# Kernel tuning notes

Hardware: AMD Instinct MI355X
Metric: run time of the kernel (lower is better)

The kernel has to match this reference:

```python
import jax, jax.numpy as jnp
import numpy as np

HIDDEN = 1024
HEADS = 16
HEAD_DIM = HIDDEN // HEADS
GAMMA = 0.5
B, S = 2, 2048


def setup_inputs() -> dict:
    key = jax.random.key(0)
    ks = jax.random.split(key, 9)
    sc = 1.0 / np.sqrt(HIDDEN)
    x = jax.random.normal(ks[0], (B, S, HIDDEN), dtype=jnp.float32)
    attn_mask = jnp.zeros((S, S), dtype=bool)  # True = masked; all-False here
    Wq = jax.random.normal(ks[1], (HIDDEN, HIDDEN), dtype=jnp.float32) * sc
    bq = jnp.zeros((HIDDEN,), dtype=jnp.float32)
    Wk = jax.random.normal(ks[2], (HIDDEN, HIDDEN), dtype=jnp.float32) * sc
    bk = jnp.zeros((HIDDEN,), dtype=jnp.float32)
    Wv = jax.random.normal(ks[3], (HIDDEN, HIDDEN), dtype=jnp.float32) * sc
    bv = jnp.zeros((HIDDEN,), dtype=jnp.float32)
    Wo = jax.random.normal(ks[4], (HIDDEN, HIDDEN), dtype=jnp.float32) * sc
    bo = jnp.zeros((HIDDEN,), dtype=jnp.float32)
    return {"x": x, "attn_mask": attn_mask, "Wq": Wq, "bq": bq,
            "Wk": Wk, "bk": bk, "Wv": Wv, "bv": bv, "Wo": Wo, "bo": bo}


def reference(x, attn_mask, Wq, bq, Wk, bk, Wv, bv, Wo, bo):
    Bn, Sn, _ = x.shape
    # projections (torch Linear: x @ W.T + b), reshape to [B, H, S, Dh]
    def proj(W, b):
        y = x @ W.T + b
        return y.reshape(Bn, Sn, HEADS, HEAD_DIM).transpose(0, 2, 1, 3)
    q, k, v = proj(Wq, bq), proj(Wk, bk), proj(Wv, bv)
    scores = jnp.einsum('bhqd,bhkd->bhqk', q, k) / np.sqrt(HEAD_DIM)
    # diversity bias: cosine similarity of raw x (F.normalize eps=1e-12)
    normed = x / jnp.maximum(jnp.linalg.norm(x, axis=-1, keepdims=True), 1e-12)
    sim = jnp.einsum('bqd,bkd->bqk', normed, normed)
    scores = scores - GAMMA * sim[:, None, :, :]
    scores = jnp.where(attn_mask[None, None, :, :], -jnp.inf, scores)
    probs = jax.nn.softmax(scores, axis=-1)
    ctx = jnp.einsum('bhqk,bhkd->bhqd', probs, v)
    ctx = ctx.transpose(0, 2, 1, 3).reshape(Bn, Sn, HIDDEN)
    return ctx @ Wo.T + bo
```

## Files before the change

kernel.cpp:

```cpp
#include <hip/hip_runtime.h>

#define HID 1024
#define SEQ 2048
#define NB 2
#define NH 16
#define HD 64

#define C1 0.1803368801111204f
#define C2 0.7213475204444817f

typedef __attribute__((ext_vector_type(8))) short bf16x8;
typedef __attribute__((ext_vector_type(8))) unsigned short u16x8;
typedef __attribute__((ext_vector_type(4))) float f32x4;

__device__ __forceinline__ unsigned short f2bf(float f) {
  unsigned u = __builtin_bit_cast(unsigned, f);
  u += 0x7fffu + ((u >> 16) & 1u);
  return (unsigned short)(u >> 16);
}
__device__ __forceinline__ float bf2f(unsigned short u) {
  return __builtin_bit_cast(float, ((unsigned)u) << 16);
}
__device__ __forceinline__ float fexp2(float x) {
  float r;
  asm("v_exp_f32 %0, %1" : "=v"(r) : "v"(x));
  return r;
}

#define GLOAD16(gsrc, ldst)                                                     \
  __builtin_amdgcn_global_load_lds(                                             \
      (const __attribute__((address_space(1))) void*)(gsrc),                    \
      (__attribute__((address_space(3))) void*)(ldst), 16, 0, 0)

__global__ __launch_bounds__(256) void prep_kernel(
    const float* __restrict__ x,
    const float* __restrict__ Wq, const float* __restrict__ Wk,
    const float* __restrict__ Wv, const float* __restrict__ Wo,
    unsigned short* __restrict__ Wb,
    unsigned short* __restrict__ xb, unsigned short* __restrict__ nxb) {
  int tid = threadIdx.x;
  if (blockIdx.x < 2048) {
    int i = blockIdx.x * 256 + tid;
    const int per = (HID * HID) / 8;
    int m = i / per;
    const float* sp = (m == 0) ? Wq : (m == 1) ? Wk : (m == 2) ? Wv : Wo;
    int j = (i - m * per) * 8;
    const float4* p = reinterpret_cast<const float4*>(sp + j);
    float4 a = p[0], b = p[1];
    u16x8 o;
    o[0] = f2bf(a.x); o[1] = f2bf(a.y); o[2] = f2bf(a.z); o[3] = f2bf(a.w);
    o[4] = f2bf(b.x); o[5] = f2bf(b.y); o[6] = f2bf(b.z); o[7] = f2bf(b.w);
    *reinterpret_cast<u16x8*>(Wb + (size_t)i * 8) = o;
  } else {
    int row = blockIdx.x - 2048;
    const float4 v = reinterpret_cast<const float4*>(x + (size_t)row * HID)[tid];
    float ss = v.x * v.x + v.y * v.y + v.z * v.z + v.w * v.w;
#pragma unroll
    for (int off = 32; off; off >>= 1) ss += __shfl_xor(ss, off, 64);
    __shared__ float wsum[4];
    if ((tid & 63) == 0) wsum[tid >> 6] = ss;
    __syncthreads();
    float tot = wsum[0] + wsum[1] + wsum[2] + wsum[3];
    float inv = 1.0f / fmaxf(sqrtf(tot), 1e-12f);
    ushort4 a, b;
    a.x = f2bf(v.x); a.y = f2bf(v.y); a.z = f2bf(v.z); a.w = f2bf(v.w);
    b.x = f2bf(v.x * inv); b.y = f2bf(v.y * inv);
    b.z = f2bf(v.z * inv); b.w = f2bf(v.w * inv);
    reinterpret_cast<ushort4*>(xb  + (size_t)row * HID)[tid] = a;
    reinterpret_cast<ushort4*>(nxb + (size_t)row * HID)[tid] = b;
  }
}

#define GEMM_K_LOOP64                                                           \
  for (int kt = 0; kt < 16; ++kt) {                                             \
    _Pragma("unroll")                                                           \
    for (int j = 0; j < 4; j++) {                                               \
      GLOAD16(Ab + (size_t)j * 32 * K + kt * 64, &As[j * 2048 + wid * 512]);    \
      GLOAD16(Bb + (size_t)j * 32 * K + kt * 64, &Bs[j * 2048 + wid * 512]);    \
    }                                                                           \
    __syncthreads();                                                            \
    _Pragma("unroll")                                                           \
    for (int h = 0; h < 2; h++) {                                               \
      bf16x8 af[4], bfr[4];                                                     \
      _Pragma("unroll")                                                         \
      for (int i = 0; i < 4; i++) {                                             \
        af[i]  = *reinterpret_cast<const bf16x8*>(                              \
            &As[(wr * 64 + i * 16 + lr) * 64 + ((((h << 2) + g) ^ (lr & 7)) << 3)]); \
        bfr[i] = *reinterpret_cast<const bf16x8*>(                              \
            &Bs[(wc * 64 + i * 16 + lr) * 64 + ((((h << 2) + g) ^ (lr & 7)) << 3)]); \
      }                                                                         \
      _Pragma("unroll")                                                         \
      for (int i = 0; i < 4; i++)                                               \
        _Pragma("unroll")                                                       \
        for (int j = 0; j < 4; j++)                                             \
          acc[i][j] = __builtin_amdgcn_mfma_f32_16x16x32_bf16(af[i], bfr[j], acc[i][j], 0, 0, 0); \
    }                                                                           \
    __syncthreads();                                                            \
  }

__global__ __launch_bounds__(256) void mega_gemm(
    const unsigned short* __restrict__ xb, const unsigned short* __restrict__ nxb,
    const unsigned short* __restrict__ Wb,
    unsigned short* __restrict__ QK, unsigned short* __restrict__ VT,
    unsigned short* __restrict__ D2,
    const float* __restrict__ bq, const float* __restrict__ bk,
    const float* __restrict__ bv, const unsigned char* __restrict__ mask) {
  const int K = HID;
  int bid = blockIdx.x;
  int mode, m0, n0;
  const unsigned short *A, *B;
  size_t zoff = 0;
  if (bid < 512) {
    mode = 0; m0 = (bid >> 4) * 128; n0 = (bid & 15) * 128;
    A = xb; B = Wb;
  } else if (bid < 768) {
    mode = 3; int t = bid - 512; m0 = (t >> 5) * 128; n0 = (t & 31) * 128;
    A = Wb + (size_t)2 * HID * HID; B = xb;
  } else {
    mode = 1; int t = bid - 768; int z = 0;
    if (t >= 136) { z = 1; t -= 136; }
    int a = (int)((sqrtf(8.0f * t + 1.0f) - 1.0f) * 0.5f);
    while (a * (a + 1) / 2 > t) a--;
    while ((a + 1) * (a + 2) / 2 <= t) a++;
    int bI = t - a * (a + 1) / 2;
    m0 = bI * 128; n0 = a * 128;
    A = nxb + (size_t)z * SEQ * HID; B = A;
    zoff = (size_t)z * SEQ * SEQ;
  }

  __shared__ __align__(16) unsigned short As[128 * 64];
  __shared__ __align__(16) unsigned short Bs[128 * 64];
  int tid = threadIdx.x, lane = tid & 63, wid = tid >> 6;
  int g = lane >> 4, lr = lane & 15;
  int wr = wid >> 1, wc = wid & 1;
  const unsigned short* Ab = A + (size_t)(m0 + wid * 8 + (lane >> 3)) * K
                             + (((lane & 7) ^ (lane >> 3)) << 3);
  const unsigned short* Bb = B + (size_t)(n0 + wid * 8 + (lane >> 3)) * K
                             + (((lane & 7) ^ (lane >> 3)) << 3);

  f32x4 acc[4][4] = {};
  GEMM_K_LOOP64

#pragma unroll
  for (int i = 0; i < 4; i++)
#pragma unroll
    for (int j = 0; j < 4; j++) {
      int col = n0 + wc * 64 + j * 16 + lr;
#pragma unroll
      for (int r = 0; r < 4; r++) {
        int row = m0 + wr * 64 + i * 16 + 4 * g + r;
        float v = acc[i][j][r];
        if (mode == 0) {
          const float* bp = (col < 1024) ? bq : bk;
          QK[(size_t)row * 2048 + col] = f2bf(v + bp[col & 1023]);
        } else if (mode == 3) {
          VT[(size_t)row * 4096 + col] = f2bf(v + bv[row]);
        } else {
          float t1 = -C2 * v + (mask[(size_t)row * SEQ + col] ? -1e30f : 0.0f);
          D2[zoff + (size_t)row * SEQ + col] = f2bf(t1);
          if (m0 != n0) {
            float t2 = -C2 * v + (mask[(size_t)col * SEQ + row] ? -1e30f : 0.0f);
            D2[zoff + (size_t)col * SEQ + row] = f2bf(t2);
          }
        }
      }
    }
}

__global__ __launch_bounds__(256) void gemm_out(
    const unsigned short* __restrict__ A, const unsigned short* __restrict__ B,
    float* __restrict__ C, const float* __restrict__ b0) {
  const int K = HID;
  __shared__ __align__(16) unsigned short As[128 * 64];
  __shared__ __align__(16) unsigned short Bs[128 * 64];
  int tid = threadIdx.x, lane = tid & 63, wid = tid >> 6;
  int g = lane >> 4, lr = lane & 15;
  int wr = wid >> 1, wc = wid & 1;
  int m0 = blockIdx.y * 128, n0 = blockIdx.x * 128;
  const unsigned short* Ab = A + (size_t)(m0 + wid * 8 + (lane >> 3)) * K
                             + (((lane & 7) ^ (lane >> 3)) << 3);
  const unsigned short* Bb = B + (size_t)(n0 + wid * 8 + (lane >> 3)) * K
                             + (((lane & 7) ^ (lane >> 3)) << 3);

  f32x4 acc[4][4] = {};
  GEMM_K_LOOP64

#pragma unroll
  for (int i = 0; i < 4; i++)
#pragma unroll
    for (int j = 0; j < 4; j++) {
      int col = n0 + wc * 64 + j * 16 + lr;
#pragma unroll
      for (int r = 0; r < 4; r++) {
        int row = m0 + wr * 64 + i * 16 + 4 * g + r;
        C[(size_t)row * HID + col] = acc[i][j][r] + b0[col];
      }
    }
}

__global__ __launch_bounds__(256, 4) void flash_kernel(
    const unsigned short* __restrict__ QK,
    const unsigned short* __restrict__ VT,
    const unsigned short* __restrict__ D2,
    unsigned short* __restrict__ ctxb) {
  int h = blockIdx.x, qt = blockIdx.y, b = blockIdx.z;
  int tid = threadIdx.x, wid = tid >> 6, lane = tid & 63;
  int g = lane >> 4, lr = lane & 15;
  __shared__ __align__(16) unsigned short Ks[2][64 * 64];
  __shared__ __align__(16) unsigned short Vt[2][64 * 64];
  const size_t ld = 2 * HID;
  const size_t bS = (size_t)b * SEQ;
  const int qbase = qt * 64 + wid * 16;

  const unsigned short* qp = QK + (bS + qbase + lr) * ld + h * HD + g * 8;
  bf16x8 qf0 = *reinterpret_cast<const bf16x8*>(qp);
  bf16x8 qf1 = *reinterpret_cast<const bf16x8*>(qp + 32);

  const int p0 = wid * 16 + (lane >> 3);
  const int key0 = ((p0 >> 5) & 1) * 32 + (((p0 >> 2) & 3) << 3)
                 + ((p0 >> 4) & 1) * 4 + (p0 & 3);
  const unsigned short* gK0 = QK + (bS + key0) * ld + HID + h * HD
                              + (((lane & 7) ^ (lane >> 3)) << 3);
  const unsigned short* gK1 = gK0 + 16 * ld;

  const unsigned short* gV0 = VT + (size_t)(h * HD + wid * 16 + (lane >> 3)) * (2 * SEQ)
                              + bS + (((lane & 7) ^ (lane >> 3)) << 3);
  const unsigned short* gV1 = gV0 + (size_t)8 * (2 * SEQ);

  const unsigned short* bD = D2 + (size_t)b * SEQ * SEQ
                             + (size_t)(qbase + lr) * SEQ + 8 * g;

  GLOAD16(gK0, &Ks[0][wid * 1024]);
  GLOAD16(gK1, &Ks[0][wid * 1024 + 512]);
  GLOAD16(gV0, &Vt[0][wid * 1024]);
  GLOAD16(gV1, &Vt[0][wid * 1024 + 512]);
  ushort4 bvc[4];
  bvc[0] = *reinterpret_cast<const ushort4*>(bD + 0);
  bvc[1] = *reinterpret_cast<const ushort4*>(bD + 4);
  bvc[2] = *reinterpret_cast<const ushort4*>(bD + 32);
  bvc[3] = *reinterpret_cast<const ushort4*>(bD + 36);
  __syncthreads();

  f32x4 acc[4] = {};
  f32x4 rsacc = {};
  const int kb0 = lr * 64 + ((g ^ (lr & 7)) << 3);
  bf16x8 ones;
#pragma unroll
  for (int i = 0; i < 8; i++) ones[i] = 0x3F80;

  for (int kt = 0; kt < 32; ++kt) {
    const int cb = kt & 1;
    const unsigned short* ks = &Ks[cb][0];
    const unsigned short* vt = &Vt[cb][0];
    ushort4 bvn[4];
    if (kt < 31) {
      GLOAD16(gK0 + (size_t)(kt + 1) * 64 * ld, &Ks[cb ^ 1][wid * 1024]);
      GLOAD16(gK1 + (size_t)(kt + 1) * 64 * ld, &Ks[cb ^ 1][wid * 1024 + 512]);
      GLOAD16(gV0 + (kt + 1) * 64, &Vt[cb ^ 1][wid * 1024]);
      GLOAD16(gV1 + (kt + 1) * 64, &Vt[cb ^ 1][wid * 1024 + 512]);
      const unsigned short* bn = bD + (kt + 1) * 64;
      bvn[0] = *reinterpret_cast<const ushort4*>(bn + 0);
      bvn[1] = *reinterpret_cast<const ushort4*>(bn + 4);
      bvn[2] = *reinterpret_cast<const ushort4*>(bn + 32);
      bvn[3] = *reinterpret_cast<const ushort4*>(bn + 36);
    }

    f32x4 s[4];
    __builtin_amdgcn_s_setprio(1);
#pragma unroll
    for (int kc = 0; kc < 4; kc++) {
      bf16x8 kf0 = *reinterpret_cast<const bf16x8*>(ks + kc * 1024 + kb0);
      bf16x8 kf1 = *reinterpret_cast<const bf16x8*>(ks + kc * 1024 + (kb0 ^ 32));
      f32x4 z = {};
      z = __builtin_amdgcn_mfma_f32_16x16x32_bf16(kf0, qf0, z, 0, 0, 0);
      s[kc] = __builtin_amdgcn_mfma_f32_16x16x32_bf16(kf1, qf1, z, 0, 0, 0);
    }
    __builtin_amdgcn_s_setprio(0);

    bf16x8 pa[2];
#pragma unroll
    for (int c2 = 0; c2 < 2; c2++) {
      float p0f = fexp2(fmaf(s[2 * c2][0], C1, bf2f(bvc[2 * c2].x)));
      float p1f = fexp2(fmaf(s[2 * c2][1], C1, bf2f(bvc[2 * c2].y)));
      float p2f = fexp2(fmaf(s[2 * c2][2], C1, bf2f(bvc[2 * c2].z)));
      float p3f = fexp2(fmaf(s[2 * c2][3], C1, bf2f(bvc[2 * c2].w)));
      float p4f = fexp2(fmaf(s[2 * c2 + 1][0], C1, bf2f(bvc[2 * c2 + 1].x)));
      float p5f = fexp2(fmaf(s[2 * c2 + 1][1], C1, bf2f(bvc[2 * c2 + 1].y)));
      float p6f = fexp2(fmaf(s[2 * c2 + 1][2], C1, bf2f(bvc[2 * c2 + 1].z)));
      float p7f = fexp2(fmaf(s[2 * c2 + 1][3], C1, bf2f(bvc[2 * c2 + 1].w)));
      uint4 W;
      W.x = __builtin_amdgcn_perm(__builtin_bit_cast(unsigned, p1f),
                                  __builtin_bit_cast(unsigned, p0f), 0x07060302u);
      W.y = __builtin_amdgcn_perm(__builtin_bit_cast(unsigned, p3f),
                                  __builtin_bit_cast(unsigned, p2f), 0x07060302u);
      W.z = __builtin_amdgcn_perm(__builtin_bit_cast(unsigned, p5f),
                                  __builtin_bit_cast(unsigned, p4f), 0x07060302u);
      W.w = __builtin_amdgcn_perm(__builtin_bit_cast(unsigned, p7f),
                                  __builtin_bit_cast(unsigned, p6f), 0x07060302u);
      pa[c2] = __builtin_bit_cast(bf16x8, W);
    }

    __builtin_amdgcn_s_setprio(1);
#pragma unroll
    for (int c2 = 0; c2 < 2; c2++) {
      rsacc = __builtin_amdgcn_mfma_f32_16x16x32_bf16(pa[c2], ones, rsacc, 0, 0, 0);
#pragma unroll
      for (int df = 0; df < 4; df++) {
        bf16x8 vf = *reinterpret_cast<const bf16x8*>(
            vt + (df * 16 + lr) * 64 + (((4 * c2 + g) ^ (lr & 7)) << 3));
        acc[df] = __builtin_amdgcn_mfma_f32_16x16x32_bf16(pa[c2], vf, acc[df], 0, 0, 0);
      }
    }
    __builtin_amdgcn_s_setprio(0);

    if (kt < 31) {
      bvc[0] = bvn[0]; bvc[1] = bvn[1]; bvc[2] = bvn[2]; bvc[3] = bvn[3];
    }
    __syncthreads();
  }
  float l0 = 1.0f / rsacc[0], l1 = 1.0f / rsacc[1];
  float l2 = 1.0f / rsacc[2], l3 = 1.0f / rsacc[3];
  unsigned short* op = ctxb + (bS + qbase + 4 * g) * HID + h * HD + lr;
#pragma unroll
  for (int df = 0; df < 4; df++) {
    op[0 * HID + df * 16] = f2bf(acc[df][0] * l0);
    op[1 * HID + df * 16] = f2bf(acc[df][1] * l1);
    op[2 * HID + df * 16] = f2bf(acc[df][2] * l2);
    op[3 * HID + df * 16] = f2bf(acc[df][3] * l3);
  }
}

extern "C" void kernel_launch(void* const* d_in, const int* in_sizes, int n_in,
                              void* d_out, int out_size, void* d_ws, size_t ws_size,
                              hipStream_t stream) {
  const float* x = (const float*)d_in[0];
  const unsigned char* mask = (const unsigned char*)d_in[1];
  const float* Wq = (const float*)d_in[2];
  const float* bq = (const float*)d_in[3];
  const float* Wk = (const float*)d_in[4];
  const float* bk = (const float*)d_in[5];
  const float* Wv = (const float*)d_in[6];
  const float* bv = (const float*)d_in[7];
  const float* Wo = (const float*)d_in[8];
  const float* bo = (const float*)d_in[9];
  float* out = (float*)d_out;

  char* ws = (char*)d_ws;
  const size_t MiB = 1024 * 1024;
  unsigned short* xb  = (unsigned short*)(ws + 0 * MiB);
  unsigned short* nxb = (unsigned short*)(ws + 8 * MiB);
  unsigned short* Wb  = (unsigned short*)(ws + 16 * MiB);
  unsigned short* QK  = (unsigned short*)(ws + 24 * MiB);
  unsigned short* VT  = (unsigned short*)(ws + 40 * MiB);
  unsigned short* D2  = (unsigned short*)(ws + 48 * MiB);
  unsigned short* ctx = (unsigned short*)(ws + 64 * MiB);

  prep_kernel<<<6144, 256, 0, stream>>>(x, Wq, Wk, Wv, Wo, Wb, xb, nxb);
  mega_gemm<<<1040, 256, 0, stream>>>(xb, nxb, Wb, QK, VT, D2, bq, bk, bv, mask);
  flash_kernel<<<dim3(NH, SEQ / 64, NB), 256, 0, stream>>>(QK, VT, D2, ctx);
  gemm_out<<<dim3(8, 32), 256, 0, stream>>>(
      ctx, Wb + (size_t)3 * HID * HID, out, bo);
}
```

Baseline: 204.7 us.

## Shrink GEMM K-tile to 32 and remap block IDs across XCDs

The shared GEMM K-loop now stages 32-wide K slices instead of 64, with a new XOR swizzle and per-wave LDS regions. This halves LDS use and may allow more resident blocks. Both mega_gemm and gemm_out also remap blockIdx so that consecutive tiles land on the same XCD (stride-8 interleave), which is meant to improve L2 reuse of shared A/B panels. The cost is twice as many barriers and a shorter MFMA run per K step.

```diff
diff --git a/kernel.cpp b/kernel.cpp
--- a/kernel.cpp
+++ b/kernel.cpp
@@ -71,30 +71,26 @@
   }
 }
 
-#define GEMM_K_LOOP64                                                           \
-  for (int kt = 0; kt < 16; ++kt) {                                             \
+#define GEMM_K_LOOP32                                                           \
+  for (int k0 = 0; k0 < K; k0 += 32) {                                          \
+    GLOAD16(Ab + k0, la);                                                       \
+    GLOAD16(Ab + 16 * K + k0, la + 512);                                        \
+    GLOAD16(Bb + k0, lb);                                                       \
+    GLOAD16(Bb + 16 * K + k0, lb + 512);                                        \
+    __syncthreads();                                                            \
+    bf16x8 af[4], bfr[4];                                                       \
     _Pragma("unroll")                                                           \
-    for (int j = 0; j < 4; j++) {                                               \
-      GLOAD16(Ab + (size_t)j * 32 * K + kt * 64, &As[j * 2048 + wid * 512]);    \
-      GLOAD16(Bb + (size_t)j * 32 * K + kt * 64, &Bs[j * 2048 + wid * 512]);    \
+    for (int i = 0; i < 4; i++) {                                               \
+      af[i]  = *reinterpret_cast<const bf16x8*>(                                \
+          &As[(wr * 64 + i * 16 + lr) * 32 + ((g ^ ((lr >> 1) & 3)) << 3)]);    \
+      bfr[i] = *reinterpret_cast<const bf16x8*>(                                \
+          &Bs[(wc * 64 + i * 16 + lr) * 32 + ((g ^ ((lr >> 1) & 3)) << 3)]);    \
     }                                                                           \
-    __syncthreads();                                                            \
     _Pragma("unroll")                                                           \
-    for (int h = 0; h < 2; h++) {                                               \
-      bf16x8 af[4], bfr[4];                                                     \
+    for (int i = 0; i < 4; i++)                                                 \
       _Pragma("unroll")                                                         \
-      for (int i = 0; i < 4; i++) {                                             \
-        af[i]  = *reinterpret_cast<const bf16x8*>(                              \
-            &As[(wr * 64 + i * 16 + lr) * 64 + ((((h << 2) + g) ^ (lr & 7)) << 3)]); \
-        bfr[i] = *reinterpret_cast<const bf16x8*>(                              \
-            &Bs[(wc * 64 + i * 16 + lr) * 64 + ((((h << 2) + g) ^ (lr & 7)) << 3)]); \
-      }                                                                         \
-      _Pragma("unroll")                                                         \
-      for (int i = 0; i < 4; i++)                                               \
-        _Pragma("unroll")                                                       \
-        for (int j = 0; j < 4; j++)                                             \
-          acc[i][j] = __builtin_amdgcn_mfma_f32_16x16x32_bf16(af[i], bfr[j], acc[i][j], 0, 0, 0); \
-    }                                                                           \
+      for (int j = 0; j < 4; j++)                                               \
+        acc[i][j] = __builtin_amdgcn_mfma_f32_16x16x32_bf16(af[i], bfr[j], acc[i][j], 0, 0, 0); \
     __syncthreads();                                                            \
   }
 
@@ -106,7 +102,7 @@
     const float* __restrict__ bq, const float* __restrict__ bk,
     const float* __restrict__ bv, const unsigned char* __restrict__ mask) {
   const int K = HID;
-  int bid = blockIdx.x;
+  int bid = (blockIdx.x & 7) * 130 + (blockIdx.x >> 3);
   int mode, m0, n0;
   const unsigned short *A, *B;
   size_t zoff = 0;
@@ -128,18 +124,20 @@
     zoff = (size_t)z * SEQ * SEQ;
   }
 
-  __shared__ __align__(16) unsigned short As[128 * 64];
-  __shared__ __align__(16) unsigned short Bs[128 * 64];
+  __shared__ __align__(16) unsigned short As[128 * 32];
+  __shared__ __align__(16) unsigned short Bs[128 * 32];
   int tid = threadIdx.x, lane = tid & 63, wid = tid >> 6;
   int g = lane >> 4, lr = lane & 15;
   int wr = wid >> 1, wc = wid & 1;
-  const unsigned short* Ab = A + (size_t)(m0 + wid * 8 + (lane >> 3)) * K
-                             + (((lane & 7) ^ (lane >> 3)) << 3);
-  const unsigned short* Bb = B + (size_t)(n0 + wid * 8 + (lane >> 3)) * K
-                             + (((lane & 7) ^ (lane >> 3)) << 3);
+  const unsigned short* Ab = A + (size_t)(m0 + wid * 32 + (lane >> 2)) * K
+                             + (((lane & 3) ^ ((lane >> 3) & 3)) << 3);
+  const unsigned short* Bb = B + (size_t)(n0 + wid * 32 + (lane >> 2)) * K
+                             + (((lane & 3) ^ ((lane >> 3) & 3)) << 3);
+  unsigned short* la = As + wid * 1024;
+  unsigned short* lb = Bs + wid * 1024;
 
   f32x4 acc[4][4] = {};
-  GEMM_K_LOOP64
+  GEMM_K_LOOP32
 
 #pragma unroll
   for (int i = 0; i < 4; i++)
@@ -171,19 +169,22 @@
     const unsigned short* __restrict__ A, const unsigned short* __restrict__ B,
     float* __restrict__ C, const float* __restrict__ b0) {
   const int K = HID;
-  __shared__ __align__(16) unsigned short As[128 * 64];
-  __shared__ __align__(16) unsigned short Bs[128 * 64];
+  __shared__ __align__(16) unsigned short As[128 * 32];
+  __shared__ __align__(16) unsigned short Bs[128 * 32];
   int tid = threadIdx.x, lane = tid & 63, wid = tid >> 6;
   int g = lane >> 4, lr = lane & 15;
   int wr = wid >> 1, wc = wid & 1;
-  int m0 = blockIdx.y * 128, n0 = blockIdx.x * 128;
-  const unsigned short* Ab = A + (size_t)(m0 + wid * 8 + (lane >> 3)) * K
-                             + (((lane & 7) ^ (lane >> 3)) << 3);
-  const unsigned short* Bb = B + (size_t)(n0 + wid * 8 + (lane >> 3)) * K
-                             + (((lane & 7) ^ (lane >> 3)) << 3);
+  int bid = (blockIdx.x & 7) * 32 + (blockIdx.x >> 3);
+  int n0 = (bid >> 5) * 128, m0 = (bid & 31) * 128;
+  const unsigned short* Ab = A + (size_t)(m0 + wid * 32 + (lane >> 2)) * K
+                             + (((lane & 3) ^ ((lane >> 3) & 3)) << 3);
+  const unsigned short* Bb = B + (size_t)(n0 + wid * 32 + (lane >> 2)) * K
+                             + (((lane & 3) ^ ((lane >> 3) & 3)) << 3);
+  unsigned short* la = As + wid * 1024;
+  unsigned short* lb = Bs + wid * 1024;
 
   f32x4 acc[4][4] = {};
-  GEMM_K_LOOP64
+  GEMM_K_LOOP32
 
 #pragma unroll
   for (int i = 0; i < 4; i++)
@@ -358,6 +359,6 @@
   prep_kernel<<<6144, 256, 0, stream>>>(x, Wq, Wk, Wv, Wo, Wb, xb, nxb);
   mega_gemm<<<1040, 256, 0, stream>>>(xb, nxb, Wb, QK, VT, D2, bq, bk, bv, mask);
   flash_kernel<<<dim3(NH, SEQ / 64, NB), 256, 0, stream>>>(QK, VT, D2, ctx);
-  gemm_out<<<dim3(8, 32), 256, 0, stream>>>(
+  gemm_out<<<256, 256, 0, stream>>>(
       ctx, Wb + (size_t)3 * HID * HID, out, bo);
 }
```

New measurement: 232.3 us. 13.5% more time.
